# Kernel tuning notes

Hardware: AMD Instinct MI355X
Metric: run time of the kernel (lower is better)

Reference implementation:

```python
import jax, jax.numpy as jnp
import numpy as np

B, N, C = 2, 2048, 1024
H = 8
DH = C // H  # head dim = 128


def setup_inputs() -> dict:
    key = jax.random.key(0)
    ks = jax.random.split(key, 10)
    s = 1.0 / np.sqrt(C)
    return {
        "inputs_q": jax.random.normal(ks[0], (B, N, C), dtype=jnp.float32),
        "inputs_kv": jax.random.normal(ks[1], (B, N, C), dtype=jnp.float32),
        "Wq": jax.random.normal(ks[2], (C, C), dtype=jnp.float32) * s,
        "bq": jnp.zeros((C,), dtype=jnp.float32),
        "Wk": jax.random.normal(ks[3], (C, C), dtype=jnp.float32) * s,
        "bk": jnp.zeros((C,), dtype=jnp.float32),
        "Wv": jax.random.normal(ks[4], (C, C), dtype=jnp.float32) * s,
        "bv": jnp.zeros((C,), dtype=jnp.float32),
        "Wo": jax.random.normal(ks[5], (C, C), dtype=jnp.float32) * s,
        "bo": jnp.zeros((C,), dtype=jnp.float32),
    }


def reference(inputs_q, inputs_kv, Wq, bq, Wk, bk, Wv, bv, Wo, bo):
    # QKV linear projections
    q = inputs_q @ Wq + bq           # [B, N, C]
    k = inputs_kv @ Wk + bk          # [B, M, C]
    v = inputs_kv @ Wv + bv          # [B, M, C]
    # split heads
    q = q.reshape(B, N, H, DH)
    k = k.reshape(B, -1, H, DH)
    v = v.reshape(B, -1, H, DH)
    # explicit attention, matching attend(): scale by 1/sqrt(head_dim)
    attn = jnp.einsum('bnhc,bmhc->bhnm', q, k) * (1.0 / np.sqrt(DH))
    normalized = jax.nn.softmax(attn, axis=-1)  # f32 softmax (inputs are f32)
    summed = jnp.einsum('bhnm,bmhd->bnhd', normalized, v)
    summed = summed.reshape(B, N, C)  # merge heads: ...n(hd)
    # output linear
    return summed @ Wo + bo
```

## Files before the change

### kernel.cpp

```cpp
#include <hip/hip_runtime.h>

typedef unsigned short u16;
typedef __bf16 bf16;
typedef __attribute__((ext_vector_type(8))) __bf16 bf16x8;
typedef __attribute__((ext_vector_type(4))) float f32x4;

#define AS1(p) ((const __attribute__((address_space(1))) void*)(p))
#define AS3(p) ((__attribute__((address_space(3))) void*)(p))

__device__ __forceinline__ u16 f2bf(float f) {
  unsigned u = __builtin_bit_cast(unsigned, f);
  u += 0x7fffu + ((u >> 16) & 1u);
  return (u16)(u >> 16);
}

static constexpr int  B_ = 2, N_ = 2048, C_ = 1024, H_ = 8, DH_ = 128;
static constexpr long SZ_IN = (long)B_ * N_ * C_;
static constexpr long SZ_W  = (long)C_ * C_;

__global__ void k_cast(const float* __restrict__ q, const float* __restrict__ kv,
                       const float* __restrict__ W0, const float* __restrict__ W1,
                       const float* __restrict__ W2, const float* __restrict__ W3,
                       u16* __restrict__ qb, u16* __restrict__ kvb,
                       u16* __restrict__ WT)
{
  __shared__ u16 t[64][65];
  int tid = threadIdx.x;
  if (blockIdx.y < 2) {
    const float* src = blockIdx.y ? kv : q;
    u16* dst = blockIdx.y ? kvb : qb;
    long i = ((long)blockIdx.x * 256 + tid) * 8;
    float4 a = *(const float4*)(src + i);
    float4 b = *(const float4*)(src + i + 4);
    uint4 v;
    v.x = f2bf(a.x) | ((unsigned)f2bf(a.y) << 16);
    v.y = f2bf(a.z) | ((unsigned)f2bf(a.w) << 16);
    v.z = f2bf(b.x) | ((unsigned)f2bf(b.y) << 16);
    v.w = f2bf(b.z) | ((unsigned)f2bf(b.w) << 16);
    *(uint4*)(dst + i) = v;
    return;
  }
  int x = blockIdx.x;
  if (x >= 1024) return;
  int z = x >> 8, tile = x & 255;
  const float* W = (z == 0) ? W0 : (z == 1) ? W1 : (z == 2) ? W2 : W3;
  u16* dst = WT + (long)z * SZ_W;
  int n0 = (tile & 15) * 64, k0 = (tile >> 4) * 64;
#pragma unroll
  for (int r = 0; r < 4; ++r) {
    int slot = r * 256 + tid;
    int row = slot >> 4, c4 = slot & 15;
    float4 a = *(const float4*)(W + (long)(k0 + row) * 1024 + n0 + c4 * 4);
    t[c4*4+0][row] = f2bf(a.x);
    t[c4*4+1][row] = f2bf(a.y);
    t[c4*4+2][row] = f2bf(a.z);
    t[c4*4+3][row] = f2bf(a.w);
  }
  __syncthreads();
#pragma unroll
  for (int r = 0; r < 4; ++r) {
    int slot = r * 256 + tid;
    int row = slot >> 4, c4 = slot & 15;
    uint2 v;
    v.x = t[row][c4*4+0] | ((unsigned)t[row][c4*4+1] << 16);
    v.y = t[row][c4*4+2] | ((unsigned)t[row][c4*4+3] << 16);
    *(uint2*)(dst + (long)(n0 + row) * 1024 + k0 + c4 * 4) = v;
  }
}

__device__ __forceinline__ void gemm_main_128x128(
    const u16* __restrict__ A, const u16* __restrict__ BT,
    u16* lA, u16* lB, int m0, int n0, int tid, f32x4 acc[4][4])
{
  int w = tid >> 6, l = tid & 63, quad = l >> 4, lm = l & 15;
  int wm = w >> 1, wn = w & 1;
  int srow = tid >> 2, schunk = tid & 3;
  int sxw = (srow >> 1) & 3;
  int sxr = (lm >> 1) & 3;
  const u16* Ag = A + (long)(m0 + srow) * 1024 + (schunk ^ sxw) * 8;
  const u16* Bg = BT + (long)(n0 + srow) * 1024 + (schunk ^ sxw) * 8;
  u16* lAw = lA + w * 512;
  u16* lBw = lB + w * 512;
  for (int kb = 0; kb < 32; ++kb) {
    const u16* Agk = Ag + kb * 32;
    const u16* Bgk = Bg + kb * 32;
    __builtin_amdgcn_global_load_lds(AS1(Agk),           AS3(lAw),        16, 0, 0);
    __builtin_amdgcn_global_load_lds(AS1(Agk + 64*1024), AS3(lAw + 2048), 16, 0, 0);
    __builtin_amdgcn_global_load_lds(AS1(Bgk),           AS3(lBw),        16, 0, 0);
    __builtin_amdgcn_global_load_lds(AS1(Bgk + 64*1024), AS3(lBw + 2048), 16, 0, 0);
    __syncthreads();
    bf16x8 af[4], bfr[4];
#pragma unroll
    for (int mi = 0; mi < 4; ++mi)
      af[mi] = *(const bf16x8*)(lA + (wm*64 + mi*16 + lm)*32 + ((quad ^ sxr))*8);
#pragma unroll
    for (int ni = 0; ni < 4; ++ni)
      bfr[ni] = *(const bf16x8*)(lB + (wn*64 + ni*16 + lm)*32 + ((quad ^ sxr))*8);
#pragma unroll
    for (int mi = 0; mi < 4; ++mi)
#pragma unroll
      for (int ni = 0; ni < 4; ++ni)
        acc[mi][ni] = __builtin_amdgcn_mfma_f32_16x16x32_bf16(af[mi], bfr[ni], acc[mi][ni], 0, 0, 0);
    __syncthreads();
  }
}

__global__ __launch_bounds__(256, 3)
void k_gemm_qkv(const u16* __restrict__ qb, const u16* __restrict__ kvb,
                const u16* __restrict__ wt,
                const float* __restrict__ bq, const float* __restrict__ bk,
                const float* __restrict__ bv,
                u16* __restrict__ Qb, u16* __restrict__ Kb, u16* __restrict__ VTb)
{
  __shared__ u16 lA[4096], lB[4096];
  int tid = threadIdx.x;
  int z = blockIdx.z;
  f32x4 acc[4][4] = {};
  int w = tid >> 6, l = tid & 63, quad = l >> 4, lm = l & 15;
  int wm = w >> 1, wn = w & 1;

  if (z == 2) {
    int m0 = blockIdx.y * 128, n0 = blockIdx.x * 128;
    gemm_main_128x128(kvb, wt + 2 * SZ_W, lA, lB, m0, n0, tid, acc);
#pragma unroll
    for (int ni = 0; ni < 4; ++ni) {
      int n = n0 + wn*64 + ni*16 + lm;
      float bb = bv[n];
      int h = n >> 7, dd = n & 127;
#pragma unroll
      for (int mi = 0; mi < 4; ++mi) {
        int mbase = m0 + wm*64 + mi*16 + quad*4;
        int bidx = mbase >> 11, nn = mbase & 2047;
        u16 o0 = f2bf(acc[mi][ni][0] + bb), o1 = f2bf(acc[mi][ni][1] + bb);
        u16 o2 = f2bf(acc[mi][ni][2] + bb), o3 = f2bf(acc[mi][ni][3] + bb);
        uint2 v; v.x = o0 | ((unsigned)o1 << 16); v.y = o2 | ((unsigned)o3 << 16);
        *(uint2*)(VTb + ((long)(bidx*8 + h)*128 + dd)*2048 + nn) = v;
      }
    }
  } else {
    const u16* X = (z == 0) ? qb : kvb;
    const float* bias = (z == 0) ? bq : bk;
    u16* dst = (z == 0) ? Qb : Kb;
    float scale = (z == 0) ? 0.08838834764831845f : 1.0f;
    int m0 = blockIdx.x * 128, n0 = blockIdx.y * 128;
    gemm_main_128x128(wt + (long)z * SZ_W, X, lA, lB, m0, n0, tid, acc);
#pragma unroll
    for (int mi = 0; mi < 4; ++mi) {
      int chb = m0 + wm*64 + mi*16 + quad*4;
      int h = chb >> 7, d = chb & 127;
      float4 bb = *(const float4*)(bias + chb);
#pragma unroll
      for (int ni = 0; ni < 4; ++ni) {
        int tok = n0 + wn*64 + ni*16 + lm;
        int bidx = tok >> 11, nn = tok & 2047;
        u16 o0 = f2bf((acc[mi][ni][0] + bb.x) * scale);
        u16 o1 = f2bf((acc[mi][ni][1] + bb.y) * scale);
        u16 o2 = f2bf((acc[mi][ni][2] + bb.z) * scale);
        u16 o3 = f2bf((acc[mi][ni][3] + bb.w) * scale);
        uint2 v; v.x = o0 | ((unsigned)o1 << 16); v.y = o2 | ((unsigned)o3 << 16);
        *(uint2*)(dst + ((long)(bidx*8 + h)*2048 + nn)*128 + d) = v;
      }
    }
  }
}

__global__ __launch_bounds__(128, 2)
void k_attn(const u16* __restrict__ Qb, const u16* __restrict__ Kb,
            const u16* __restrict__ VTb, u16* __restrict__ Sout)
{
  __shared__ u16 smem[18560];
  u16*   lP    = smem + 16384;
  float* lStat = (float*)(smem + 18432);

  int tid = threadIdx.x;
  int w = tid >> 6, l = tid & 63, quad = l >> 4, lm = l & 15;
  int kh = w;
  int bh = blockIdx.x;
  int q0 = blockIdx.y * 32;
  const u16* Qg = Qb + ((long)bh * 2048 + q0) * 128;
  const u16* Kg = Kb + (long)bh * 2048 * 128;
  const u16* Vg = VTb + (long)bh * 128 * 2048;
  u16* lPw = lP + w * 1024;

  bf16x8 qf[2][4];
#pragma unroll
  for (int mi = 0; mi < 2; ++mi)
#pragma unroll
    for (int kk = 0; kk < 4; ++kk)
      qf[mi][kk] = *(const bf16x8*)(Qg + (long)(mi*16 + lm)*128 + kk*32 + quad*8);

  f32x4 accO[2][8] = {};
  float sumP[2][4] = {};

  auto stage = [&](int tt) {
    u16* dstb = smem + (kh*2 + (tt & 1)) * 4096;
#pragma unroll
    for (int j = 0; j < 8; ++j) {
      int s = j*64 + l;
      int r = s >> 4, c = s & 15;
      __builtin_amdgcn_global_load_lds(
          AS1(Kg + (long)(kh*1024 + tt*32 + r)*128 + ((c ^ (r & 7)) * 8)),
          AS3(dstb + j*512), 16, 0, 0);
    }
  };

  stage(0);

#pragma unroll 1
  for (int t = 0; t < 32; ++t) {
    __syncthreads();
    stage(t + 1);

    int k0 = kh*1024 + t*32;
    bf16x8 vf[8];
#pragma unroll
    for (int ni = 0; ni < 8; ++ni)
      vf[ni] = *(const bf16x8*)(Vg + (long)(ni*16 + lm)*2048 + k0 + quad*8);

    const u16* bk = smem + (kh*2 + (t & 1)) * 4096;
    f32x4 accS[2][2] = {};
#pragma unroll
    for (int kk = 0; kk < 4; ++kk)
#pragma unroll
      for (int ni = 0; ni < 2; ++ni) {
        bf16x8 kf = *(const bf16x8*)(bk + ((ni*16 + lm)*16 + (((kk*4 + quad) ^ (lm & 7))))*8);
#pragma unroll
        for (int mi = 0; mi < 2; ++mi)
          accS[mi][ni] = __builtin_amdgcn_mfma_f32_16x16x32_bf16(qf[mi][kk], kf, accS[mi][ni], 0, 0, 0);
      }

#pragma unroll
    for (int mi = 0; mi < 2; ++mi)
#pragma unroll
      for (int r = 0; r < 4; ++r) {
        int R = mi*16 + quad*4 + r;
        int xr = (quad*2 + (r >> 1)) & 3;
#pragma unroll
        for (int ni = 0; ni < 2; ++ni) {
          float p = __expf(accS[mi][ni][r]);
          sumP[mi][r] += p;
          int ch = ni*2 + (lm >> 3);
          lPw[(R*4 + (ch ^ xr))*8 + (lm & 7)] = f2bf(p);
        }
      }

    bf16x8 pf[2];
#pragma unroll
    for (int mi = 0; mi < 2; ++mi)
      pf[mi] = *(const bf16x8*)(lPw + ((mi*16 + lm)*4 + (quad ^ ((lm >> 1) & 3)))*8);

#pragma unroll
    for (int ni = 0; ni < 8; ++ni)
#pragma unroll
      for (int mi = 0; mi < 2; ++mi)
        accO[mi][ni] = __builtin_amdgcn_mfma_f32_16x16x32_bf16(pf[mi], vf[ni], accO[mi][ni], 0, 0, 0);
  }

#pragma unroll
  for (int mi = 0; mi < 2; ++mi)
#pragma unroll
    for (int r = 0; r < 4; ++r) {
      float s = sumP[mi][r];
      s += __shfl_xor(s, 1);
      s += __shfl_xor(s, 2);
      s += __shfl_xor(s, 4);
      s += __shfl_xor(s, 8);
      lStat[w*32 + mi*16 + quad*4 + r] = s;
    }

  float* lO = (float*)smem;
  __syncthreads();
  if (w == 1) {
#pragma unroll
    for (int mi = 0; mi < 2; ++mi)
#pragma unroll
      for (int ni = 0; ni < 8; ++ni)
#pragma unroll
        for (int r = 0; r < 4; ++r)
          lO[(mi*16 + quad*4 + r)*128 + ni*16 + lm] = accO[mi][ni][r];
  }
  __syncthreads();
  if (w == 0) {
    int b = bh >> 3, h = bh & 7;
#pragma unroll
    for (int mi = 0; mi < 2; ++mi)
#pragma unroll
      for (int r = 0; r < 4; ++r) {
        int R = mi*16 + quad*4 + r;
        float linv = 1.f / (lStat[R] + lStat[32 + R]);
#pragma unroll
        for (int ni = 0; ni < 8; ++ni) {
          float v = (accO[mi][ni][r] + lO[R*128 + ni*16 + lm]) * linv;
          Sout[((long)(b*2048 + q0 + R))*1024 + h*128 + ni*16 + lm] = f2bf(v);
        }
      }
  }
}

__global__ __launch_bounds__(256, 3)
void k_gemm_out(const u16* __restrict__ S, const u16* __restrict__ WoT,
                const float* __restrict__ bo, float* __restrict__ out)
{
  __shared__ u16 lA[4096], lB[4096];
  int tid = threadIdx.x;
  int m0 = blockIdx.x * 128, n0 = blockIdx.y * 128;
  f32x4 acc[4][4] = {};
  gemm_main_128x128(WoT, S, lA, lB, m0, n0, tid, acc);

  int w = tid >> 6, l = tid & 63, quad = l >> 4, lm = l & 15;
  int wm = w >> 1, wn = w & 1;
#pragma unroll
  for (int mi = 0; mi < 4; ++mi) {
    int chb = m0 + wm*64 + mi*16 + quad*4;
    float4 bb = *(const float4*)(bo + chb);
#pragma unroll
    for (int ni = 0; ni < 4; ++ni) {
      int tok = n0 + wn*64 + ni*16 + lm;
      float4 v;
      v.x = acc[mi][ni][0] + bb.x;
      v.y = acc[mi][ni][1] + bb.y;
      v.z = acc[mi][ni][2] + bb.z;
      v.w = acc[mi][ni][3] + bb.w;
      *(float4*)(out + (long)tok * 1024 + chb) = v;
    }
  }
}

extern "C" void kernel_launch(void* const* d_in, const int* in_sizes, int n_in,
                              void* d_out, int out_size, void* d_ws, size_t ws_size,
                              hipStream_t stream)
{
  const float* inq  = (const float*)d_in[0];
  const float* inkv = (const float*)d_in[1];
  const float* Wq = (const float*)d_in[2];
  const float* bq = (const float*)d_in[3];
  const float* Wk = (const float*)d_in[4];
  const float* bk = (const float*)d_in[5];
  const float* Wv = (const float*)d_in[6];
  const float* bv = (const float*)d_in[7];
  const float* Wo = (const float*)d_in[8];
  const float* bo = (const float*)d_in[9];

  u16* ws   = (u16*)d_ws;
  u16* ABUF = ws;
  u16* KVB  = ws + SZ_IN;
  u16* WT   = ws + 2 * SZ_IN;
  u16* Qb   = WT + 4 * SZ_W;
  u16* Kb   = Qb + SZ_IN;
  u16* VTb  = Kb + SZ_IN;

  k_cast    <<<dim3(2048, 3),   256, 0, stream>>>(inq, inkv, Wq, Wk, Wv, Wo, ABUF, KVB, WT);
  k_gemm_qkv<<<dim3(8, 32, 3),  256, 0, stream>>>(ABUF, KVB, WT, bq, bk, bv, Qb, Kb, VTb);
  k_attn    <<<dim3(16, 64),    128, 0, stream>>>(Qb, Kb, VTb, ABUF);
  k_gemm_out<<<dim3(8, 32),     256, 0, stream>>>(ABUF, WT + 3 * SZ_W, bo, (float*)d_out);
}
```

Before: 243.7 us.

## Split attention block across four waves: two key halves times two query halves

The attention kernel now launches 256 threads per block instead of 128. Each wave handles 16 query rows and one half of the keys, where before each wave handled 32 rows. This halves the per-wave accumulator and register footprint and raises wave-level parallelism and occupancy (launch bounds 256,4). The trade-off is that each V fragment is loaded from global memory by twice as many waves, and the K tile staging is shared across the two query waves.

```diff
diff --git a/kernel.cpp b/kernel.cpp
--- a/kernel.cpp
+++ b/kernel.cpp
@@ -164,7 +164,7 @@
   }
 }
 
-__global__ __launch_bounds__(128, 2)
+__global__ __launch_bounds__(256, 4)
 void k_attn(const u16* __restrict__ Qb, const u16* __restrict__ Kb,
             const u16* __restrict__ VTb, u16* __restrict__ Sout)
 {
@@ -174,33 +174,32 @@
 
   int tid = threadIdx.x;
   int w = tid >> 6, l = tid & 63, quad = l >> 4, lm = l & 15;
-  int kh = w;
+  int wk = w >> 1;
+  int wq = w & 1;
   int bh = blockIdx.x;
   int q0 = blockIdx.y * 32;
-  const u16* Qg = Qb + ((long)bh * 2048 + q0) * 128;
+  const u16* Qg = Qb + ((long)bh * 2048 + q0 + wq * 16) * 128;
   const u16* Kg = Kb + (long)bh * 2048 * 128;
   const u16* Vg = VTb + (long)bh * 128 * 2048;
-  u16* lPw = lP + w * 1024;
-
-  bf16x8 qf[2][4];
-#pragma unroll
-  for (int mi = 0; mi < 2; ++mi)
-#pragma unroll
-    for (int kk = 0; kk < 4; ++kk)
-      qf[mi][kk] = *(const bf16x8*)(Qg + (long)(mi*16 + lm)*128 + kk*32 + quad*8);
-
-  f32x4 accO[2][8] = {};
-  float sumP[2][4] = {};
+  u16* lPw = lP + w * 512;
+
+  bf16x8 qf[4];
+#pragma unroll
+  for (int kk = 0; kk < 4; ++kk)
+    qf[kk] = *(const bf16x8*)(Qg + (long)lm * 128 + kk*32 + quad*8);
+
+  f32x4 accO[8] = {};
+  float sumP[4] = {};
 
   auto stage = [&](int tt) {
-    u16* dstb = smem + (kh*2 + (tt & 1)) * 4096;
-#pragma unroll
-    for (int j = 0; j < 8; ++j) {
-      int s = j*64 + l;
+    u16* dstb = smem + (wk*2 + (tt & 1)) * 4096;
+#pragma unroll
+    for (int j = 0; j < 4; ++j) {
+      int s = j*128 + wq*64 + l;
       int r = s >> 4, c = s & 15;
       __builtin_amdgcn_global_load_lds(
-          AS1(Kg + (long)(kh*1024 + tt*32 + r)*128 + ((c ^ (r & 7)) * 8)),
-          AS3(dstb + j*512), 16, 0, 0);
+          AS1(Kg + (long)(wk*1024 + tt*32 + r)*128 + ((c ^ (r & 7)) * 8)),
+          AS3(dstb + j*1024 + wq*512), 16, 0, 0);
     }
   };
 
@@ -211,89 +210,75 @@
     __syncthreads();
     stage(t + 1);
 
-    int k0 = kh*1024 + t*32;
+    int k0 = wk*1024 + t*32;
     bf16x8 vf[8];
 #pragma unroll
     for (int ni = 0; ni < 8; ++ni)
       vf[ni] = *(const bf16x8*)(Vg + (long)(ni*16 + lm)*2048 + k0 + quad*8);
 
-    const u16* bk = smem + (kh*2 + (t & 1)) * 4096;
-    f32x4 accS[2][2] = {};
+    const u16* bk = smem + (wk*2 + (t & 1)) * 4096;
+    f32x4 accS[2] = {};
 #pragma unroll
     for (int kk = 0; kk < 4; ++kk)
 #pragma unroll
       for (int ni = 0; ni < 2; ++ni) {
         bf16x8 kf = *(const bf16x8*)(bk + ((ni*16 + lm)*16 + (((kk*4 + quad) ^ (lm & 7))))*8);
-#pragma unroll
-        for (int mi = 0; mi < 2; ++mi)
-          accS[mi][ni] = __builtin_amdgcn_mfma_f32_16x16x32_bf16(qf[mi][kk], kf, accS[mi][ni], 0, 0, 0);
-      }
-
-#pragma unroll
-    for (int mi = 0; mi < 2; ++mi)
-#pragma unroll
-      for (int r = 0; r < 4; ++r) {
-        int R = mi*16 + quad*4 + r;
-        int xr = (quad*2 + (r >> 1)) & 3;
-#pragma unroll
-        for (int ni = 0; ni < 2; ++ni) {
-          float p = __expf(accS[mi][ni][r]);
-          sumP[mi][r] += p;
-          int ch = ni*2 + (lm >> 3);
-          lPw[(R*4 + (ch ^ xr))*8 + (lm & 7)] = f2bf(p);
-        }
-      }
-
-    bf16x8 pf[2];
-#pragma unroll
-    for (int mi = 0; mi < 2; ++mi)
-      pf[mi] = *(const bf16x8*)(lPw + ((mi*16 + lm)*4 + (quad ^ ((lm >> 1) & 3)))*8);
+        accS[ni] = __builtin_amdgcn_mfma_f32_16x16x32_bf16(qf[kk], kf, accS[ni], 0, 0, 0);
+      }
+
+#pragma unroll
+    for (int r = 0; r < 4; ++r) {
+      int R = quad*4 + r;
+      int xr = (quad*2 + (r >> 1)) & 3;
+#pragma unroll
+      for (int ni = 0; ni < 2; ++ni) {
+        float p = __expf(accS[ni][r]);
+        sumP[r] += p;
+        int ch = ni*2 + (lm >> 3);
+        lPw[(R*4 + (ch ^ xr))*8 + (lm & 7)] = f2bf(p);
+      }
+    }
+
+    bf16x8 pf = *(const bf16x8*)(lPw + (lm*4 + (quad ^ ((lm >> 1) & 3)))*8);
 
 #pragma unroll
     for (int ni = 0; ni < 8; ++ni)
-#pragma unroll
-      for (int mi = 0; mi < 2; ++mi)
-        accO[mi][ni] = __builtin_amdgcn_mfma_f32_16x16x32_bf16(pf[mi], vf[ni], accO[mi][ni], 0, 0, 0);
-  }
-
-#pragma unroll
-  for (int mi = 0; mi < 2; ++mi)
-#pragma unroll
-    for (int r = 0; r < 4; ++r) {
-      float s = sumP[mi][r];
-      s += __shfl_xor(s, 1);
-      s += __shfl_xor(s, 2);
-      s += __shfl_xor(s, 4);
-      s += __shfl_xor(s, 8);
-      lStat[w*32 + mi*16 + quad*4 + r] = s;
-    }
+      accO[ni] = __builtin_amdgcn_mfma_f32_16x16x32_bf16(pf, vf[ni], accO[ni], 0, 0, 0);
+  }
+
+#pragma unroll
+  for (int r = 0; r < 4; ++r) {
+    float s = sumP[r];
+    s += __shfl_xor(s, 1);
+    s += __shfl_xor(s, 2);
+    s += __shfl_xor(s, 4);
+    s += __shfl_xor(s, 8);
+    lStat[w*16 + quad*4 + r] = s;
+  }
 
   float* lO = (float*)smem;
   __syncthreads();
-  if (w == 1) {
-#pragma unroll
-    for (int mi = 0; mi < 2; ++mi)
-#pragma unroll
-      for (int ni = 0; ni < 8; ++ni)
-#pragma unroll
-        for (int r = 0; r < 4; ++r)
-          lO[(mi*16 + quad*4 + r)*128 + ni*16 + lm] = accO[mi][ni][r];
+  if (wk == 1) {
+#pragma unroll
+    for (int ni = 0; ni < 8; ++ni)
+#pragma unroll
+      for (int r = 0; r < 4; ++r)
+        lO[(wq*16 + quad*4 + r)*128 + ni*16 + lm] = accO[ni][r];
   }
   __syncthreads();
-  if (w == 0) {
+  if (wk == 0) {
     int b = bh >> 3, h = bh & 7;
 #pragma unroll
-    for (int mi = 0; mi < 2; ++mi)
-#pragma unroll
-      for (int r = 0; r < 4; ++r) {
-        int R = mi*16 + quad*4 + r;
-        float linv = 1.f / (lStat[R] + lStat[32 + R]);
-#pragma unroll
-        for (int ni = 0; ni < 8; ++ni) {
-          float v = (accO[mi][ni][r] + lO[R*128 + ni*16 + lm]) * linv;
-          Sout[((long)(b*2048 + q0 + R))*1024 + h*128 + ni*16 + lm] = f2bf(v);
-        }
-      }
+    for (int r = 0; r < 4; ++r) {
+      int R = quad*4 + r;
+      int Rg = wq*16 + R;
+      float linv = 1.f / (lStat[wq*16 + R] + lStat[(2 + wq)*16 + R]);
+#pragma unroll
+      for (int ni = 0; ni < 8; ++ni) {
+        float v = (accO[ni][r] + lO[Rg*128 + ni*16 + lm]) * linv;
+        Sout[((long)(b*2048 + q0 + Rg))*1024 + h*128 + ni*16 + lm] = f2bf(v);
+      }
+    }
   }
 }
 
@@ -351,6 +336,6 @@
 
   k_cast    <<<dim3(2048, 3),   256, 0, stream>>>(inq, inkv, Wq, Wk, Wv, Wo, ABUF, KVB, WT);
   k_gemm_qkv<<<dim3(8, 32, 3),  256, 0, stream>>>(ABUF, KVB, WT, bq, bk, bv, Qb, Kb, VTb);
-  k_attn    <<<dim3(16, 64),    128, 0, stream>>>(Qb, Kb, VTb, ABUF);
+  k_attn    <<<dim3(16, 64),    256, 0, stream>>>(Qb, Kb, VTb, ABUF);
   k_gemm_out<<<dim3(8, 32),     256, 0, stream>>>(ABUF, WT + 3 * SZ_W, bo, (float*)d_out);
 }
```

After: 298.3 us. 1.22x slower.
